# Kernel optimization log

Hardware: AMD Instinct MI355X
Metric: run time of the kernel (lower is better)

Reference implementation:

```python
import jax, jax.numpy as jnp
import numpy as np

# dims: batch, tokens, channels, heads, head_dim, slices, context_slices, context_dim
B, N, C, H, D, G, SC, DC = 2, 32768, 256, 8, 32, 32, 64, 32
EPS_SLICE = 1e-5


def _ln(x, g, b):
    m = x.mean(-1, keepdims=True)
    v = ((x - m) ** 2).mean(-1, keepdims=True)
    return (x - m) * jax.lax.rsqrt(v + 1e-5) * g + b


def setup_inputs() -> dict:
    key = jax.random.key(0)
    ks = jax.random.split(key, 16)
    w = lambda k, s: jax.random.normal(k, s, jnp.float32) * 0.02
    return dict(
        fx=jax.random.normal(ks[0], (B, N, C), jnp.float32),
        context=jax.random.normal(ks[1], (B, H, SC, DC), jnp.float32),
        ln1_g=jnp.ones((C,), jnp.float32), ln1_b=jnp.zeros((C,), jnp.float32),
        Wfx=w(ks[2], (C, H * D)), bfx=jnp.zeros((H * D,), jnp.float32),
        Wx=w(ks[3], (C, H * D)), bx=jnp.zeros((H * D,), jnp.float32),
        Wslice=w(ks[4], (D, G)), bslice=jnp.zeros((G,), jnp.float32),
        temperature=0.5 * jnp.ones((1, H, 1, 1), jnp.float32),
        Wq=w(ks[5], (D, D)), Wk=w(ks[6], (D, D)), Wv=w(ks[7], (D, D)),
        Wcq=w(ks[8], (D, D)), bcq=jnp.zeros((D,), jnp.float32),
        Wck=w(ks[9], (DC, D)), bck=jnp.zeros((D,), jnp.float32),
        Wcv=w(ks[10], (DC, D)), bcv=jnp.zeros((D,), jnp.float32),
        state_mixing=jnp.zeros((), jnp.float32),
        Wout=w(ks[11], (H * D, C)), bout=jnp.zeros((C,), jnp.float32),
        ln2_g=jnp.ones((C,), jnp.float32), ln2_b=jnp.zeros((C,), jnp.float32),
        Wm1=w(ks[12], (C, 4 * C)), bm1=jnp.zeros((4 * C,), jnp.float32),
        Wm2=w(ks[13], (4 * C, C)), bm2=jnp.zeros((C,), jnp.float32),
    )


def reference(fx, context, ln1_g, ln1_b, Wfx, bfx, Wx, bx, Wslice, bslice,
              temperature, Wq, Wk, Wv, Wcq, bcq, Wck, bck, Wcv, bcv,
              state_mixing, Wout, bout, ln2_g, ln2_b, Wm1, bm1, Wm2, bm2):
    # --- GALE attention on pre-normed input (Transolver physics attention + cross) ---
    x = _ln(fx, ln1_g, ln1_b)
    fxm = (x @ Wfx + bfx).reshape(B, N, H, D).transpose(0, 2, 1, 3)  # b h n d
    xm = (x @ Wx + bx).reshape(B, N, H, D).transpose(0, 2, 1, 3)    # b h n d
    # slice weights: softmax over slices with learnable per-head temperature
    sw = jax.nn.softmax((xm @ Wslice + bslice) / temperature, axis=-1)  # b h n g
    norm = sw.sum(2)  # b h g
    st = jnp.einsum('bhnd,bhng->bhgd', fxm, sw) / (norm + EPS_SLICE)[..., None]
    scale = D ** -0.5
    # self-attention among slice tokens (no bias on q/k/v)
    q, k, v = st @ Wq, st @ Wk, st @ Wv
    sattn = jax.nn.softmax(jnp.einsum('bhgd,bhmd->bhgm', q, k) * scale, axis=-1)
    self_tok = jnp.einsum('bhgm,bhmd->bhgd', sattn, v)
    # cross-attention of slice tokens onto geometry/global context
    cq = st @ Wcq + bcq
    ck = context @ Wck + bck
    cv = context @ Wcv + bcv
    cattn = jax.nn.softmax(jnp.einsum('bhgd,bhsd->bhgs', cq, ck) * scale, axis=-1)
    cross_tok = jnp.einsum('bhgs,bhsd->bhgd', cattn, cv)
    # sigmoid-gated mix
    mw = jax.nn.sigmoid(state_mixing)
    ost = mw * self_tok + (1.0 - mw) * cross_tok
    # de-slice back to tokens and output-project
    out = jnp.einsum('bhgd,bhng->bhnd', ost, sw)
    out = out.transpose(0, 2, 1, 3).reshape(B, N, H * D) @ Wout + bout
    fx = fx + out  # residual 1
    # --- MLP block ---
    h = _ln(fx, ln2_g, ln2_b)
    fx = fx + (jax.nn.gelu(h @ Wm1 + bm1, approximate=False) @ Wm2 + bm2)
    return fx
```

## Files before the change

kernel.cpp:

```cpp
#include <hip/hip_runtime.h>
#include <hip/hip_bf16.h>

#define BATCH 2
#define NTOK  32768
#define CH    256
#define NH    8
#define HDIM  32
#define NG    32
#define NSC   64
#define NDC   32

typedef __attribute__((ext_vector_type(8))) short short8v;
typedef __attribute__((ext_vector_type(4))) short short4v;
typedef __attribute__((ext_vector_type(4))) float f32x4;

static __device__ __forceinline__ short f2bf(float f) {
    __hip_bfloat16 h = __float2bfloat16(f);
    return __builtin_bit_cast(short, h);
}
static __device__ __forceinline__ float bf2f(short s) {
    return __bfloat162float(__builtin_bit_cast(__hip_bfloat16, s));
}

__global__ __launch_bounds__(256) void kconv_transpose(
    const float* __restrict__ in, __hip_bfloat16* __restrict__ out,
    int K, int N)
{
    __shared__ float t[32][33];
    const int nb = N >> 5;
    const int bk = blockIdx.x / nb;
    const int bn = blockIdx.x % nb;
    const int c = threadIdx.x & 31, r0 = threadIdx.x >> 5;
    #pragma unroll
    for (int i = 0; i < 4; ++i) {
        const int r = r0 + i * 8;
        t[r][c] = in[(long)(bk * 32 + r) * N + bn * 32 + c];
    }
    __syncthreads();
    #pragma unroll
    for (int i = 0; i < 4; ++i) {
        const int r = r0 + i * 8;
        out[(long)(bn * 32 + r) * K + bk * 32 + c] = __float2bfloat16(t[c][r]);
    }
}

__global__ __launch_bounds__(256) void kcomb(
    const float* __restrict__ Wx, const float* __restrict__ bx,
    const float* __restrict__ Wsl, const float* __restrict__ bsl,
    __hip_bfloat16* __restrict__ wcat2, float* __restrict__ bcomb)
{
    __shared__ float wcol[32];
    const int hc = blockIdx.x;
    const int h = hc >> 5, g = hc & 31;
    const int tid = threadIdx.x;
    if (tid < 32) wcol[tid] = Wsl[tid * 32 + g];
    __syncthreads();
    float a = 0.f;
    #pragma unroll
    for (int d = 0; d < 32; ++d) a += Wx[tid * 256 + h * 32 + d] * wcol[d];
    wcat2[(long)hc * 256 + tid] = __float2bfloat16(a);
    if (tid == 0) {
        float s = bsl[g];
        #pragma unroll
        for (int d = 0; d < 32; ++d) s += bx[h * 32 + d] * wcol[d];
        bcomb[hc] = s;
    }
}

__global__ __launch_bounds__(256, 2) void k1_mfma(
    const float* __restrict__ fx,
    const float* __restrict__ g1, const float* __restrict__ b1,
    const __hip_bfloat16* __restrict__ wcat,
    const float* __restrict__ bfx, const float* __restrict__ bcomb,
    const float* __restrict__ temp,
    __hip_bfloat16* __restrict__ fxm_o, __hip_bfloat16* __restrict__ sw_o)
{
    __shared__ __align__(16) char lds[65536];
    const int tid = threadIdx.x;
    const int lane = tid & 63, wid = tid >> 6;
    const long tok0 = (long)blockIdx.x * 64;
    const int col = lane & 15, kq = lane >> 4;
    const int swz = (col & 7) << 4;
    const int ep = ((kq * 16) ^ swz) & 48;
    const int e0 = (swz & 64) | ep;
    const int e1 = ((swz & 64) ^ 64) | ep;
    const int ab0 = col * 512 + e0, ab1 = col * 512 + e1;

    {
        const float4 gv = *reinterpret_cast<const float4*>(g1 + lane * 4);
        const float4 bv = *reinterpret_cast<const float4*>(b1 + lane * 4);
        for (int tt = 0; tt < 16; ++tt) {
            const int r = wid * 16 + tt;
            const float4 v = *reinterpret_cast<const float4*>(fx + (tok0 + r) * 256 + lane * 4);
            float s = v.x + v.y + v.z + v.w;
            float s2 = v.x * v.x + v.y * v.y + v.z * v.z + v.w * v.w;
            #pragma unroll
            for (int off = 32; off; off >>= 1) {
                s  += __shfl_xor(s,  off);
                s2 += __shfl_xor(s2, off);
            }
            const float mean = s * (1.f / 256.f);
            const float rs = rsqrtf(s2 * (1.f / 256.f) - mean * mean + 1e-5f);
            short4v o;
            o[0] = f2bf((v.x - mean) * rs * gv.x + bv.x);
            o[1] = f2bf((v.y - mean) * rs * gv.y + bv.y);
            o[2] = f2bf((v.z - mean) * rs * gv.z + bv.z);
            o[3] = f2bf((v.w - mean) * rs * gv.w + bv.w);
            const int addr = r * 512 + ((lane * 8) ^ ((r & 7) << 4));
            *reinterpret_cast<short4v*>(lds + addr) = o;
        }
    }
    __syncthreads();

    f32x4 acc[4][8];
    #pragma unroll
    for (int mt = 0; mt < 4; ++mt)
        #pragma unroll
        for (int nt = 0; nt < 8; ++nt) acc[mt][nt] = (f32x4){0.f, 0.f, 0.f, 0.f};

    const short* wp = reinterpret_cast<const short*>(wcat) + (wid * 128 + col) * 256 + kq * 8;
    #pragma unroll 2
    for (int j = 0; j < 4; ++j) {
        short8v a0[4], a1[4];
        #pragma unroll
        for (int mt = 0; mt < 4; ++mt) {
            a0[mt] = *reinterpret_cast<const short8v*>(lds + mt * 8192 + j * 128 + ab0);
            a1[mt] = *reinterpret_cast<const short8v*>(lds + mt * 8192 + j * 128 + ab1);
        }
        #pragma unroll
        for (int nt = 0; nt < 8; ++nt) {
            const short8v b0 = *reinterpret_cast<const short8v*>(wp + nt * 4096 + j * 64);
            const short8v b1 = *reinterpret_cast<const short8v*>(wp + nt * 4096 + j * 64 + 32);
            #pragma unroll
            for (int mt = 0; mt < 4; ++mt) {
                acc[mt][nt] = __builtin_amdgcn_mfma_f32_16x16x32_bf16(a0[mt], b0, acc[mt][nt], 0, 0, 0);
                acc[mt][nt] = __builtin_amdgcn_mfma_f32_16x16x32_bf16(a1[mt], b1, acc[mt][nt], 0, 0, 0);
            }
        }
    }
    __syncthreads();

    #pragma unroll
    for (int nt = 0; nt < 8; ++nt) {
        const int c = wid * 128 + nt * 16 + col;
        const float bb = (c < 256) ? bfx[c] : bcomb[c - 256];
        #pragma unroll
        for (int mt = 0; mt < 4; ++mt) {
            #pragma unroll
            for (int r = 0; r < 4; ++r) {
                const int row = mt * 16 + kq * 4 + r;
                const int byte = row * 1024 + ((c * 2) ^ ((row & 7) << 4));
                *reinterpret_cast<short*>(lds + byte) = f2bf(acc[mt][nt][r] + bb);
            }
        }
    }
    __syncthreads();

    #pragma unroll
    for (int it = 0; it < 8; ++it) {
        const int idx = it * 256 + tid;
        const int row = idx >> 5, ch = idx & 31;
        const short8v val = *reinterpret_cast<const short8v*>(
            lds + row * 1024 + ((ch * 16) ^ ((row & 7) << 4)));
        *reinterpret_cast<short8v*>(
            reinterpret_cast<short*>(fxm_o) + (tok0 + row) * 256 + ch * 8) = val;
    }

    #pragma unroll
    for (int pp = 0; pp < 2; ++pp) {
        const int p = pp * 256 + tid;
        const int t = p >> 3, h = p & 7;
        const float it_ = 1.f / temp[h];
        float lg[32];
        #pragma unroll
        for (int g = 0; g < 32; ++g) {
            const int byte = t * 1024 + (((256 + h * 32 + g) * 2) ^ ((t & 7) << 4));
            lg[g] = bf2f(*reinterpret_cast<const short*>(lds + byte)) * it_;
        }
        float mx = -1e30f;
        #pragma unroll
        for (int g = 0; g < 32; ++g) mx = fmaxf(mx, lg[g]);
        float ssum = 0.f;
        #pragma unroll
        for (int g = 0; g < 32; ++g) { lg[g] = __expf(lg[g] - mx); ssum += lg[g]; }
        const float inv = 1.f / ssum;
        #pragma unroll
        for (int g = 0; g < 32; ++g) {
            const int byte = t * 1024 + (((256 + h * 32 + g) * 2) ^ ((t & 7) << 4));
            *reinterpret_cast<short*>(lds + byte) = f2bf(lg[g] * inv);
        }
    }
    __syncthreads();

    #pragma unroll
    for (int it = 0; it < 8; ++it) {
        const int idx = it * 256 + tid;
        const int row = idx >> 5, ch = idx & 31;
        const short8v val = *reinterpret_cast<const short8v*>(
            lds + row * 1024 + ((512 + ch * 16) ^ ((row & 7) << 4)));
        *reinterpret_cast<short8v*>(
            reinterpret_cast<short*>(sw_o) + (tok0 + row) * 256 + ch * 8) = val;
    }
}

__global__ __launch_bounds__(256) void k2_st_partial(
    const __hip_bfloat16* __restrict__ fxm, const __hip_bfloat16* __restrict__ sw,
    float* __restrict__ pst, float* __restrict__ pn)
{
    __shared__ float psum[4][32][32];
    __shared__ float pns[4][32];
    const int tid = threadIdx.x, wid = tid >> 6, lane = tid & 63;
    const int blk = blockIdx.x;
    const int bh = blk >> 5, chunk = blk & 31;
    const int b = bh >> 3, h = bh & 7;
    const long rbase = (long)b * NTOK + (long)chunk * 1024 + wid * 256;
    const int gB = lane >> 3, dB = lane & 7;
    const short* sp = reinterpret_cast<const short*>(sw) + rbase * 256 + h * 32 + gB * 4;
    const short* fp = reinterpret_cast<const short*>(fxm) + rbase * 256 + h * 32 + dB * 4;

    float acc[4][4];
    float nacc[4];
    #pragma unroll
    for (int i = 0; i < 4; ++i) {
        nacc[i] = 0.f;
        #pragma unroll
        for (int j = 0; j < 4; ++j) acc[i][j] = 0.f;
    }

    #pragma unroll 4
    for (int r = 0; r < 256; ++r) {
        const short4v s4 = *reinterpret_cast<const short4v*>(sp + r * 256);
        const short4v f4 = *reinterpret_cast<const short4v*>(fp + r * 256);
        float sg[4], fd[4];
        #pragma unroll
        for (int i = 0; i < 4; ++i) { sg[i] = bf2f(s4[i]); fd[i] = bf2f(f4[i]); }
        #pragma unroll
        for (int gg = 0; gg < 4; ++gg) {
            nacc[gg] += sg[gg];
            #pragma unroll
            for (int dd = 0; dd < 4; ++dd) acc[gg][dd] += sg[gg] * fd[dd];
        }
    }

    #pragma unroll
    for (int gg = 0; gg < 4; ++gg) {
        #pragma unroll
        for (int dd = 0; dd < 4; ++dd)
            psum[wid][gB * 4 + gg][dB * 4 + dd] = acc[gg][dd];
        if (dB == 0) pns[wid][gB * 4 + gg] = nacc[gg];
    }
    __syncthreads();

    for (int i = tid; i < 1024; i += 256) {
        const int g = i >> 5, d = i & 31;
        pst[(long)blk * 1024 + i] =
            psum[0][g][d] + psum[1][g][d] + psum[2][g][d] + psum[3][g][d];
    }
    if (tid < 32)
        pn[blk * 32 + tid] = pns[0][tid] + pns[1][tid] + pns[2][tid] + pns[3][tid];
}

__global__ __launch_bounds__(256) void k3_slice_attn(
    const float* __restrict__ pst, const float* __restrict__ pn,
    const float* __restrict__ ctx,
    const float* __restrict__ Wq, const float* __restrict__ Wk, const float* __restrict__ Wv,
    const float* __restrict__ Wcq, const float* __restrict__ bcq,
    const float* __restrict__ Wck, const float* __restrict__ bck,
    const float* __restrict__ Wcv, const float* __restrict__ bcv,
    const float* __restrict__ mix, __hip_bfloat16* __restrict__ ostT_o)
{
    __shared__ float st[1024], qm[1024], km[1024], vm[1024], cqm[1024];
    __shared__ float ckm[2048], cvm[2048], attn[2048], stok[1024], nb[32];
    const int tid = threadIdx.x;
    const int bh = blockIdx.x;

    if (tid < 32) {
        float s = 0.f;
        for (int c = 0; c < 32; ++c) s += pn[(bh * 32 + c) * 32 + tid];
        nb[tid] = s;
    }
    __syncthreads();
    for (int i = tid; i < 1024; i += 256) {
        float s = 0.f;
        for (int c = 0; c < 32; ++c) s += pst[(long)(bh * 32 + c) * 1024 + i];
        st[i] = s / (nb[i >> 5] + 1e-5f);
    }
    __syncthreads();

    for (int i = tid; i < 1024; i += 256) {
        const int g = i >> 5, d = i & 31;
        float aq = 0.f, ak = 0.f, av = 0.f, ac = bcq[d];
        #pragma unroll
        for (int e = 0; e < 32; ++e) {
            const float s = st[g * 32 + e];
            aq += s * Wq[e * 32 + d];
            ak += s * Wk[e * 32 + d];
            av += s * Wv[e * 32 + d];
            ac += s * Wcq[e * 32 + d];
        }
        qm[i] = aq; km[i] = ak; vm[i] = av; cqm[i] = ac;
    }
    const float* cbp = ctx + (long)bh * (NSC * NDC);
    for (int i = tid; i < 2048; i += 256) {
        const int s_ = i >> 5, d = i & 31;
        float w1 = bck[d], w2 = bcv[d];
        #pragma unroll
        for (int e = 0; e < 32; ++e) {
            const float cval = cbp[s_ * 32 + e];
            w1 += cval * Wck[e * 32 + d];
            w2 += cval * Wcv[e * 32 + d];
        }
        ckm[i] = w1; cvm[i] = w2;
    }
    __syncthreads();

    const float scale = 0.17677669529663687f;
    for (int i = tid; i < 1024; i += 256) {
        const int g = i >> 5, m = i & 31;
        float a = 0.f;
        #pragma unroll
        for (int d = 0; d < 32; ++d) a += qm[g * 32 + d] * km[m * 32 + d];
        attn[i] = a * scale;
    }
    __syncthreads();
    if (tid < 32) {
        float mx = -1e30f;
        for (int m = 0; m < 32; ++m) mx = fmaxf(mx, attn[tid * 32 + m]);
        float s = 0.f;
        for (int m = 0; m < 32; ++m) { const float e = expf(attn[tid * 32 + m] - mx); attn[tid * 32 + m] = e; s += e; }
        const float inv = 1.f / s;
        for (int m = 0; m < 32; ++m) attn[tid * 32 + m] *= inv;
    }
    __syncthreads();
    for (int i = tid; i < 1024; i += 256) {
        const int g = i >> 5, d = i & 31;
        float a = 0.f;
        #pragma unroll
        for (int m = 0; m < 32; ++m) a += attn[g * 32 + m] * vm[m * 32 + d];
        stok[i] = a;
    }
    __syncthreads();
    for (int i = tid; i < 2048; i += 256) {
        const int g = i >> 6, s_ = i & 63;
        float a = 0.f;
        #pragma unroll
        for (int d = 0; d < 32; ++d) a += cqm[g * 32 + d] * ckm[s_ * 32 + d];
        attn[i] = a * scale;
    }
    __syncthreads();
    if (tid < 32) {
        float mx = -1e30f;
        for (int m = 0; m < 64; ++m) mx = fmaxf(mx, attn[tid * 64 + m]);
        float s = 0.f;
        for (int m = 0; m < 64; ++m) { const float e = expf(attn[tid * 64 + m] - mx); attn[tid * 64 + m] = e; s += e; }
        const float inv = 1.f / s;
        for (int m = 0; m < 64; ++m) attn[tid * 64 + m] *= inv;
    }
    __syncthreads();
    const float mw = 1.f / (1.f + expf(-mix[0]));
    for (int i = tid; i < 1024; i += 256) {
        const int g = i >> 5, d = i & 31;
        float a = 0.f;
        #pragma unroll
        for (int s_ = 0; s_ < 64; ++s_) a += attn[g * 64 + s_] * cvm[s_ * 32 + d];
        const float val = mw * stok[i] + (1.f - mw) * a;
        ostT_o[(long)bh * 1024 + d * 32 + g] = __float2bfloat16(val);
    }
}

__global__ __launch_bounds__(512, 4) void k45_fused(
    const __hip_bfloat16* __restrict__ sw, const __hip_bfloat16* __restrict__ ostT,
    const __hip_bfloat16* __restrict__ woutt, const float* __restrict__ bout,
    const float* __restrict__ fx,
    const float* __restrict__ g2, const float* __restrict__ b2,
    const __hip_bfloat16* __restrict__ w1t, const float* __restrict__ bm1,
    const __hip_bfloat16* __restrict__ w2t, const float* __restrict__ bm2,
    float* __restrict__ out)
{
    __shared__ __align__(16) char lds[65536];
    const int tid = threadIdx.x;
    const int lane = tid & 63, wid = tid >> 6;
    const long tok0 = (long)blockIdx.x * 64;
    const int b = (int)(tok0 >> 15);
    const int col = lane & 15, kq = lane >> 4;
    const int swz = (col & 7) << 4;
    const int ep = ((kq * 16) ^ swz) & 48;
    const int e0 = (swz & 64) | ep;
    const int e1 = ((swz & 64) ^ 64) | ep;
    const int ab0 = col * 512 + e0, ab1 = col * 512 + e1;
    const int cb0 = col * 256 + e0, cb1 = col * 256 + e1;

    #pragma unroll
    for (int it = 0; it < 4; ++it) {
        const int idx = it * 512 + tid;
        const int row = idx >> 5, ch = idx & 31;
        const short8v val = *reinterpret_cast<const short8v*>(
            reinterpret_cast<const short*>(sw) + (tok0 + row) * 256 + ch * 8);
        *reinterpret_cast<short8v*>(lds + row * 512 + ((ch * 16) ^ ((row & 7) << 4))) = val;
    }
    __syncthreads();

    {
        f32x4 accal[4][2];
        const int abh = col * 512 + (((wid * 64) | (kq * 16)) ^ swz);
        short8v a[4];
        #pragma unroll
        for (int mt = 0; mt < 4; ++mt)
            a[mt] = *reinterpret_cast<const short8v*>(lds + mt * 8192 + abh);
        #pragma unroll
        for (int nt = 0; nt < 2; ++nt) {
            const int d = nt * 16 + col;
            const short8v bfr = *reinterpret_cast<const short8v*>(
                reinterpret_cast<const short*>(ostT) + ((b * 8 + wid) * 32 + d) * 32 + kq * 8);
            #pragma unroll
            for (int mt = 0; mt < 4; ++mt) {
                accal[mt][nt] = (f32x4){0.f, 0.f, 0.f, 0.f};
                accal[mt][nt] = __builtin_amdgcn_mfma_f32_16x16x32_bf16(
                    a[mt], bfr, accal[mt][nt], 0, 0, 0);
            }
        }
        #pragma unroll
        for (int nt = 0; nt < 2; ++nt) {
            const int cc = wid * 32 + nt * 16 + col;
            #pragma unroll
            for (int mt = 0; mt < 4; ++mt) {
                #pragma unroll
                for (int r = 0; r < 4; ++r) {
                    const int row = mt * 16 + kq * 4 + r;
                    const int byte = 32768 + row * 512 + ((cc * 2) ^ ((row & 7) << 4));
                    *reinterpret_cast<short*>(lds + byte) = f2bf(accal[mt][nt][r]);
                }
            }
        }
    }
    __syncthreads();

    f32x4 acc[4][2];
    #pragma unroll
    for (int mt = 0; mt < 4; ++mt)
        #pragma unroll
        for (int nt = 0; nt < 2; ++nt) acc[mt][nt] = (f32x4){0.f, 0.f, 0.f, 0.f};

    {
        const short* wp = reinterpret_cast<const short*>(woutt) + (wid * 32 + col) * 256 + kq * 8;
        #pragma unroll 2
        for (int j = 0; j < 4; ++j) {
            short8v a0[4], a1[4];
            #pragma unroll
            for (int mt = 0; mt < 4; ++mt) {
                a0[mt] = *reinterpret_cast<const short8v*>(lds + 32768 + mt * 8192 + j * 128 + ab0);
                a1[mt] = *reinterpret_cast<const short8v*>(lds + 32768 + mt * 8192 + j * 128 + ab1);
            }
            #pragma unroll
            for (int nt = 0; nt < 2; ++nt) {
                const short8v b0 = *reinterpret_cast<const short8v*>(wp + nt * 4096 + j * 64);
                const short8v b1 = *reinterpret_cast<const short8v*>(wp + nt * 4096 + j * 64 + 32);
                #pragma unroll
                for (int mt = 0; mt < 4; ++mt) {
                    acc[mt][nt] = __builtin_amdgcn_mfma_f32_16x16x32_bf16(a0[mt], b0, acc[mt][nt], 0, 0, 0);
                    acc[mt][nt] = __builtin_amdgcn_mfma_f32_16x16x32_bf16(a1[mt], b1, acc[mt][nt], 0, 0, 0);
                }
            }
        }
    }

    __syncthreads();
    float* lf = reinterpret_cast<float*>(lds);
    #pragma unroll
    for (int nt = 0; nt < 2; ++nt) {
        const int c = wid * 32 + nt * 16 + col;
        const float bb = bout[c];
        #pragma unroll
        for (int mt = 0; mt < 4; ++mt) {
            #pragma unroll
            for (int r = 0; r < 4; ++r) {
                const int row = mt * 16 + kq * 4 + r;
                lf[row * 256 + c] = acc[mt][nt][r] + bb;
            }
        }
    }
    __syncthreads();

    f32x4 oa[8];
    short4v aout[8];
    {
        const float4 gv = *reinterpret_cast<const float4*>(g2 + lane * 4);
        const float4 bv = *reinterpret_cast<const float4*>(b2 + lane * 4);
        #pragma unroll
        for (int tt = 0; tt < 8; ++tt) {
            const int r = wid * 8 + tt;
            const float4 l4 = *reinterpret_cast<const float4*>(lf + r * 256 + lane * 4);
            const float4 f4 = *reinterpret_cast<const float4*>(fx + (tok0 + r) * 256 + lane * 4);
            const float vx = l4.x + f4.x, vy = l4.y + f4.y;
            const float vz = l4.z + f4.z, vw = l4.w + f4.w;
            oa[tt] = (f32x4){vx, vy, vz, vw};
            float s = vx + vy + vz + vw;
            float s2 = vx * vx + vy * vy + vz * vz + vw * vw;
            #pragma unroll
            for (int off = 32; off; off >>= 1) {
                s  += __shfl_xor(s,  off);
                s2 += __shfl_xor(s2, off);
            }
            const float mean = s * (1.f / 256.f);
            const float rs = rsqrtf(s2 * (1.f / 256.f) - mean * mean + 1e-5f);
            aout[tt][0] = f2bf((vx - mean) * rs * gv.x + bv.x);
            aout[tt][1] = f2bf((vy - mean) * rs * gv.y + bv.y);
            aout[tt][2] = f2bf((vz - mean) * rs * gv.z + bv.z);
            aout[tt][3] = f2bf((vw - mean) * rs * gv.w + bv.w);
        }
    }
    __syncthreads();
    #pragma unroll
    for (int tt = 0; tt < 8; ++tt) {
        const int r = wid * 8 + tt;
        const int addr = r * 512 + ((lane * 8) ^ ((r & 7) << 4));
        *reinterpret_cast<short4v*>(lds + addr) = aout[tt];
    }
    __syncthreads();

    const int n0 = wid * 32;
    const int h0 = wid * 16;
    const short* w1s = reinterpret_cast<const short*>(w1t) + (h0 + col) * 256 + kq * 8;
    const short* w2s = reinterpret_cast<const short*>(w2t) + (n0 + col) * 1024 + kq * 8;

    f32x4 accO[4][2];
    #pragma unroll
    for (int mt = 0; mt < 4; ++mt)
        #pragma unroll
        for (int nt = 0; nt < 2; ++nt) accO[mt][nt] = (f32x4){0.f, 0.f, 0.f, 0.f};

    for (int ch = 0; ch < 8; ++ch) {
        f32x4 accP[4];
        #pragma unroll
        for (int mt = 0; mt < 4; ++mt) accP[mt] = (f32x4){0.f, 0.f, 0.f, 0.f};

        #pragma unroll 2
        for (int j = 0; j < 4; ++j) {
            const short8v b0 = *reinterpret_cast<const short8v*>(w1s + ch * 32768 + j * 64);
            const short8v b1 = *reinterpret_cast<const short8v*>(w1s + ch * 32768 + j * 64 + 32);
            #pragma unroll
            for (int mt = 0; mt < 4; ++mt) {
                const short8v a0 = *reinterpret_cast<const short8v*>(lds + mt * 8192 + j * 128 + ab0);
                const short8v a1 = *reinterpret_cast<const short8v*>(lds + mt * 8192 + j * 128 + ab1);
                accP[mt] = __builtin_amdgcn_mfma_f32_16x16x32_bf16(a0, b0, accP[mt], 0, 0, 0);
                accP[mt] = __builtin_amdgcn_mfma_f32_16x16x32_bf16(a1, b1, accP[mt], 0, 0, 0);
            }
        }

        __syncthreads();
        {
            const float b1v = bm1[ch * 128 + h0 + col];
            const int k2i2 = (h0 + col) * 2;
            #pragma unroll
            for (int mt = 0; mt < 4; ++mt) {
                #pragma unroll
                for (int r = 0; r < 4; ++r) {
                    float m = accP[mt][r] + b1v;
                    const float u = __builtin_fmaf(0.044715f * m, m * m, m);
                    const float e = __expf(-1.5957691216057308f * u);
                    m = m * __builtin_amdgcn_rcpf(1.f + e);
                    const int row = mt * 16 + kq * 4 + r;
                    const int byte = 32768 + row * 256 + (k2i2 ^ ((row & 7) << 4));
                    *reinterpret_cast<short*>(lds + byte) = f2bf(m);
                }
            }
        }
        __syncthreads();

        #pragma unroll 2
        for (int j = 0; j < 2; ++j) {
            short8v b20[2], b21[2];
            #pragma unroll
            for (int nt = 0; nt < 2; ++nt) {
                b20[nt] = *reinterpret_cast<const short8v*>(w2s + nt * 16384 + ch * 128 + j * 64);
                b21[nt] = *reinterpret_cast<const short8v*>(w2s + nt * 16384 + ch * 128 + j * 64 + 32);
            }
            #pragma unroll
            for (int mt = 0; mt < 4; ++mt) {
                const short8v x0 = *reinterpret_cast<const short8v*>(lds + 32768 + mt * 4096 + j * 128 + cb0);
                const short8v x1 = *reinterpret_cast<const short8v*>(lds + 32768 + mt * 4096 + j * 128 + cb1);
                #pragma unroll
                for (int nt = 0; nt < 2; ++nt) {
                    accO[mt][nt] = __builtin_amdgcn_mfma_f32_16x16x32_bf16(x0, b20[nt], accO[mt][nt], 0, 0, 0);
                    accO[mt][nt] = __builtin_amdgcn_mfma_f32_16x16x32_bf16(x1, b21[nt], accO[mt][nt], 0, 0, 0);
                }
            }
        }
    }

    __syncthreads();
    #pragma unroll
    for (int nt = 0; nt < 2; ++nt) {
        const int c = n0 + nt * 16 + col;
        const float b2v = bm2[c];
        #pragma unroll
        for (int mt = 0; mt < 4; ++mt) {
            #pragma unroll
            for (int r = 0; r < 4; ++r) {
                const int row = mt * 16 + kq * 4 + r;
                lf[row * 256 + c] = accO[mt][nt][r] + b2v;
            }
        }
    }
    __syncthreads();
    #pragma unroll
    for (int tt = 0; tt < 8; ++tt) {
        const int r = wid * 8 + tt;
        const float4 m4 = *reinterpret_cast<const float4*>(lf + r * 256 + lane * 4);
        float4 o;
        o.x = oa[tt][0] + m4.x;
        o.y = oa[tt][1] + m4.y;
        o.z = oa[tt][2] + m4.z;
        o.w = oa[tt][3] + m4.w;
        *reinterpret_cast<float4*>(out + (tok0 + r) * 256 + lane * 4) = o;
    }
}

extern "C" void kernel_launch(void* const* d_in, const int* in_sizes, int n_in,
                              void* d_out, int out_size, void* d_ws, size_t ws_size,
                              hipStream_t stream)
{
    const float* fx   = (const float*)d_in[0];
    const float* ctx  = (const float*)d_in[1];
    const float* g1   = (const float*)d_in[2];
    const float* b1   = (const float*)d_in[3];
    const float* Wfx  = (const float*)d_in[4];
    const float* bfx  = (const float*)d_in[5];
    const float* Wx   = (const float*)d_in[6];
    const float* bx   = (const float*)d_in[7];
    const float* Wsl  = (const float*)d_in[8];
    const float* bsl  = (const float*)d_in[9];
    const float* temp = (const float*)d_in[10];
    const float* Wq   = (const float*)d_in[11];
    const float* Wk   = (const float*)d_in[12];
    const float* Wv   = (const float*)d_in[13];
    const float* Wcq  = (const float*)d_in[14];
    const float* bcq  = (const float*)d_in[15];
    const float* Wck  = (const float*)d_in[16];
    const float* bck  = (const float*)d_in[17];
    const float* Wcv  = (const float*)d_in[18];
    const float* bcv  = (const float*)d_in[19];
    const float* mix  = (const float*)d_in[20];
    const float* Wout = (const float*)d_in[21];
    const float* bout = (const float*)d_in[22];
    const float* g2   = (const float*)d_in[23];
    const float* b2   = (const float*)d_in[24];
    const float* Wm1  = (const float*)d_in[25];
    const float* bm1  = (const float*)d_in[26];
    const float* Wm2  = (const float*)d_in[27];
    const float* bm2  = (const float*)d_in[28];
    float* out = (float*)d_out;

    char* ws = (char*)d_ws;
    __hip_bfloat16* fxm  = (__hip_bfloat16*)ws;
    __hip_bfloat16* sw   = (__hip_bfloat16*)(ws + (size_t)33554432);
    float* pst = (float*)(ws + (size_t)67108864);
    float* pn  = (float*)(ws + (size_t)69206016);
    __hip_bfloat16* ostT  = (__hip_bfloat16*)(ws + (size_t)69271552);
    __hip_bfloat16* wcat  = (__hip_bfloat16*)(ws + (size_t)69304320);
    __hip_bfloat16* woutt = (__hip_bfloat16*)(ws + (size_t)69566464);
    __hip_bfloat16* w1t   = (__hip_bfloat16*)(ws + (size_t)69697536);
    __hip_bfloat16* w2t   = (__hip_bfloat16*)(ws + (size_t)70221824);
    float* bcomb          = (float*)(ws + (size_t)70746112);

    kconv_transpose<<<64,  256, 0, stream>>>(Wfx, wcat,  256, 256);
    kcomb<<<256, 256, 0, stream>>>(Wx, bx, Wsl, bsl, wcat + 65536, bcomb);
    kconv_transpose<<<64,  256, 0, stream>>>(Wout, woutt, 256, 256);
    kconv_transpose<<<256, 256, 0, stream>>>(Wm1, w1t,    256, 1024);
    kconv_transpose<<<256, 256, 0, stream>>>(Wm2, w2t,    1024, 256);

    k1_mfma<<<1024, 256, 0, stream>>>(fx, g1, b1, wcat, bfx, bcomb, temp,
                                      fxm, sw);
    k2_st_partial<<<512, 256, 0, stream>>>(fxm, sw, pst, pn);
    k3_slice_attn<<<16, 256, 0, stream>>>(pst, pn, ctx, Wq, Wk, Wv,
                                          Wcq, bcq, Wck, bck, Wcv, bcv, mix, ostT);
    k45_fused<<<1024, 512, 0, stream>>>(sw, ostT, woutt, bout, fx,
                                        g2, b2, w1t, bm1, w2t, bm2, out);
}
```

Baseline: 329.3 us.

## Widen MLP hidden chunk to 256 and spill residual to output buffer

The fused MLP kernel now processes the 1024-wide hidden dimension in 4 chunks of 256 instead of 8 chunks of 128. Each wave computes two 16-column tiles of the first GEMM, reusing the A fragments it loads from LDS across both. The hidden activations are stored with a new swizzled LDS layout that the second GEMM reads with the same addressing as the first. The residual sum (fx + attention output) is written to global output early and re-read at the end instead of being held in 32 registers, which lowers register pressure at the cost of extra global traffic.

```diff
diff --git a/kernel.cpp b/kernel.cpp
--- a/kernel.cpp
+++ b/kernel.cpp
@@ -388,7 +388,6 @@
     const int e0 = (swz & 64) | ep;
     const int e1 = ((swz & 64) ^ 64) | ep;
     const int ab0 = col * 512 + e0, ab1 = col * 512 + e1;
-    const int cb0 = col * 256 + e0, cb1 = col * 256 + e1;
 
     #pragma unroll
     for (int it = 0; it < 4; ++it) {
@@ -481,7 +480,6 @@
     }
     __syncthreads();
 
-    f32x4 oa[8];
     short4v aout[8];
     {
         const float4 gv = *reinterpret_cast<const float4*>(g2 + lane * 4);
@@ -491,11 +489,12 @@
             const int r = wid * 8 + tt;
             const float4 l4 = *reinterpret_cast<const float4*>(lf + r * 256 + lane * 4);
             const float4 f4 = *reinterpret_cast<const float4*>(fx + (tok0 + r) * 256 + lane * 4);
-            const float vx = l4.x + f4.x, vy = l4.y + f4.y;
-            const float vz = l4.z + f4.z, vw = l4.w + f4.w;
-            oa[tt] = (f32x4){vx, vy, vz, vw};
-            float s = vx + vy + vz + vw;
-            float s2 = vx * vx + vy * vy + vz * vz + vw * vw;
+            float4 oa;
+            oa.x = l4.x + f4.x; oa.y = l4.y + f4.y;
+            oa.z = l4.z + f4.z; oa.w = l4.w + f4.w;
+            *reinterpret_cast<float4*>(out + (tok0 + r) * 256 + lane * 4) = oa;
+            float s = oa.x + oa.y + oa.z + oa.w;
+            float s2 = oa.x * oa.x + oa.y * oa.y + oa.z * oa.z + oa.w * oa.w;
             #pragma unroll
             for (int off = 32; off; off >>= 1) {
                 s  += __shfl_xor(s,  off);
@@ -503,10 +502,10 @@
             }
             const float mean = s * (1.f / 256.f);
             const float rs = rsqrtf(s2 * (1.f / 256.f) - mean * mean + 1e-5f);
-            aout[tt][0] = f2bf((vx - mean) * rs * gv.x + bv.x);
-            aout[tt][1] = f2bf((vy - mean) * rs * gv.y + bv.y);
-            aout[tt][2] = f2bf((vz - mean) * rs * gv.z + bv.z);
-            aout[tt][3] = f2bf((vw - mean) * rs * gv.w + bv.w);
+            aout[tt][0] = f2bf((oa.x - mean) * rs * gv.x + bv.x);
+            aout[tt][1] = f2bf((oa.y - mean) * rs * gv.y + bv.y);
+            aout[tt][2] = f2bf((oa.z - mean) * rs * gv.z + bv.z);
+            aout[tt][3] = f2bf((oa.w - mean) * rs * gv.w + bv.w);
         }
     }
     __syncthreads();
@@ -519,9 +518,9 @@
     __syncthreads();
 
     const int n0 = wid * 32;
-    const int h0 = wid * 16;
-    const short* w1s = reinterpret_cast<const short*>(w1t) + (h0 + col) * 256 + kq * 8;
+    const short* w1s = reinterpret_cast<const short*>(w1t) + (n0 + col) * 256 + kq * 8;
     const short* w2s = reinterpret_cast<const short*>(w2t) + (n0 + col) * 1024 + kq * 8;
+    const int gsw = (kq & 1) << 6;
 
     f32x4 accO[4][2];
     #pragma unroll
@@ -529,38 +528,50 @@
         #pragma unroll
         for (int nt = 0; nt < 2; ++nt) accO[mt][nt] = (f32x4){0.f, 0.f, 0.f, 0.f};
 
-    for (int ch = 0; ch < 8; ++ch) {
-        f32x4 accP[4];
-        #pragma unroll
-        for (int mt = 0; mt < 4; ++mt) accP[mt] = (f32x4){0.f, 0.f, 0.f, 0.f};
+    for (int ch = 0; ch < 4; ++ch) {
+        f32x4 accP[4][2];
+        #pragma unroll
+        for (int mt = 0; mt < 4; ++mt)
+            #pragma unroll
+            for (int nt = 0; nt < 2; ++nt) accP[mt][nt] = (f32x4){0.f, 0.f, 0.f, 0.f};
 
         #pragma unroll 2
         for (int j = 0; j < 4; ++j) {
-            const short8v b0 = *reinterpret_cast<const short8v*>(w1s + ch * 32768 + j * 64);
-            const short8v b1 = *reinterpret_cast<const short8v*>(w1s + ch * 32768 + j * 64 + 32);
+            short8v a0[4], a1[4];
             #pragma unroll
             for (int mt = 0; mt < 4; ++mt) {
-                const short8v a0 = *reinterpret_cast<const short8v*>(lds + mt * 8192 + j * 128 + ab0);
-                const short8v a1 = *reinterpret_cast<const short8v*>(lds + mt * 8192 + j * 128 + ab1);
-                accP[mt] = __builtin_amdgcn_mfma_f32_16x16x32_bf16(a0, b0, accP[mt], 0, 0, 0);
-                accP[mt] = __builtin_amdgcn_mfma_f32_16x16x32_bf16(a1, b1, accP[mt], 0, 0, 0);
+                a0[mt] = *reinterpret_cast<const short8v*>(lds + mt * 8192 + j * 128 + ab0);
+                a1[mt] = *reinterpret_cast<const short8v*>(lds + mt * 8192 + j * 128 + ab1);
+            }
+            #pragma unroll
+            for (int nt = 0; nt < 2; ++nt) {
+                const short8v b0 = *reinterpret_cast<const short8v*>(
+                    w1s + ch * 65536 + nt * 4096 + j * 64);
+                const short8v b1 = *reinterpret_cast<const short8v*>(
+                    w1s + ch * 65536 + nt * 4096 + j * 64 + 32);
+                #pragma unroll
+                for (int mt = 0; mt < 4; ++mt) {
+                    accP[mt][nt] = __builtin_amdgcn_mfma_f32_16x16x32_bf16(a0[mt], b0, accP[mt][nt], 0, 0, 0);
+                    accP[mt][nt] = __builtin_amdgcn_mfma_f32_16x16x32_bf16(a1[mt], b1, accP[mt][nt], 0, 0, 0);
+                }
             }
         }
 
         __syncthreads();
-        {
-            const float b1v = bm1[ch * 128 + h0 + col];
-            const int k2i2 = (h0 + col) * 2;
+        #pragma unroll
+        for (int nt = 0; nt < 2; ++nt) {
+            const float b1v = bm1[ch * 256 + n0 + nt * 16 + col];
+            const int k2i2 = (n0 + nt * 16 + col) * 2;
             #pragma unroll
             for (int mt = 0; mt < 4; ++mt) {
                 #pragma unroll
                 for (int r = 0; r < 4; ++r) {
-                    float m = accP[mt][r] + b1v;
+                    float m = accP[mt][nt][r] + b1v;
                     const float u = __builtin_fmaf(0.044715f * m, m * m, m);
                     const float e = __expf(-1.5957691216057308f * u);
                     m = m * __builtin_amdgcn_rcpf(1.f + e);
-                    const int row = mt * 16 + kq * 4 + r;
-                    const int byte = 32768 + row * 256 + (k2i2 ^ ((row & 7) << 4));
+                    const int byte = 32768 + kq * 2048 + mt * 8192 + r * 512
+                                     + (k2i2 ^ (gsw + r * 16));
                     *reinterpret_cast<short*>(lds + byte) = f2bf(m);
                 }
             }
@@ -568,21 +579,23 @@
         __syncthreads();
 
         #pragma unroll 2
-        for (int j = 0; j < 2; ++j) {
-            short8v b20[2], b21[2];
+        for (int j = 0; j < 4; ++j) {
+            short8v a0[4], a1[4];
+            #pragma unroll
+            for (int mt = 0; mt < 4; ++mt) {
+                a0[mt] = *reinterpret_cast<const short8v*>(lds + 32768 + mt * 8192 + j * 128 + ab0);
+                a1[mt] = *reinterpret_cast<const short8v*>(lds + 32768 + mt * 8192 + j * 128 + ab1);
+            }
             #pragma unroll
             for (int nt = 0; nt < 2; ++nt) {
-                b20[nt] = *reinterpret_cast<const short8v*>(w2s + nt * 16384 + ch * 128 + j * 64);
-                b21[nt] = *reinterpret_cast<const short8v*>(w2s + nt * 16384 + ch * 128 + j * 64 + 32);
-            }
-            #pragma unroll
-            for (int mt = 0; mt < 4; ++mt) {
-                const short8v x0 = *reinterpret_cast<const short8v*>(lds + 32768 + mt * 4096 + j * 128 + cb0);
-                const short8v x1 = *reinterpret_cast<const short8v*>(lds + 32768 + mt * 4096 + j * 128 + cb1);
+                const short8v b0 = *reinterpret_cast<const short8v*>(
+                    w2s + nt * 16384 + ch * 256 + j * 64);
+                const short8v b1 = *reinterpret_cast<const short8v*>(
+                    w2s + nt * 16384 + ch * 256 + j * 64 + 32);
                 #pragma unroll
-                for (int nt = 0; nt < 2; ++nt) {
-                    accO[mt][nt] = __builtin_amdgcn_mfma_f32_16x16x32_bf16(x0, b20[nt], accO[mt][nt], 0, 0, 0);
-                    accO[mt][nt] = __builtin_amdgcn_mfma_f32_16x16x32_bf16(x1, b21[nt], accO[mt][nt], 0, 0, 0);
+                for (int mt = 0; mt < 4; ++mt) {
+                    accO[mt][nt] = __builtin_amdgcn_mfma_f32_16x16x32_bf16(a0[mt], b0, accO[mt][nt], 0, 0, 0);
+                    accO[mt][nt] = __builtin_amdgcn_mfma_f32_16x16x32_bf16(a1[mt], b1, accO[mt][nt], 0, 0, 0);
                 }
             }
         }
@@ -607,12 +620,12 @@
     for (int tt = 0; tt < 8; ++tt) {
         const int r = wid * 8 + tt;
         const float4 m4 = *reinterpret_cast<const float4*>(lf + r * 256 + lane * 4);
+        const long gidx = (tok0 + r) * 256 + lane * 4;
+        const float4 oa = *reinterpret_cast<const float4*>(out + gidx);
         float4 o;
-        o.x = oa[tt][0] + m4.x;
-        o.y = oa[tt][1] + m4.y;
-        o.z = oa[tt][2] + m4.z;
-        o.w = oa[tt][3] + m4.w;
-        *reinterpret_cast<float4*>(out + (tok0 + r) * 256 + lane * 4) = o;
+        o.x = oa.x + m4.x; o.y = oa.y + m4.y;
+        o.z = oa.z + m4.z; o.w = oa.w + m4.w;
+        *reinterpret_cast<float4*>(out + gidx) = o;
     }
 }
 
```

Measured after the change: 321.4 us. 2.4% less time.

## Widen k1 and k2 to 512 threads, merge weight transposes, tune k45 occupancy

Applied to the files above, without the earlier changes.

Four weight-transpose launches become one kernel that dispatches on block index. k1_mfma and k2_st_partial move from 256 to 512 threads per block, halving each wave's share of the output tiles and rows, which raises wave-level parallelism and lowers per-thread register pressure. k45_fused gets an explicit waves-per-EU attribute and its inner GEMM loops drop from unroll 2 to unroll 1, to hold occupancy. The risks are more LDS reduction traffic in k2 and less instruction-level overlap in k45 from the reduced unrolling.

```diff
diff --git a/kernel.cpp b/kernel.cpp
--- a/kernel.cpp
+++ b/kernel.cpp
@@ -22,15 +22,15 @@
     return __bfloat162float(__builtin_bit_cast(__hip_bfloat16, s));
 }
 
-__global__ __launch_bounds__(256) void kconv_transpose(
+static __device__ __forceinline__ void transpose_tile(
     const float* __restrict__ in, __hip_bfloat16* __restrict__ out,
-    int K, int N)
+    int K, int N, int blk, int tid)
 {
     __shared__ float t[32][33];
     const int nb = N >> 5;
-    const int bk = blockIdx.x / nb;
-    const int bn = blockIdx.x % nb;
-    const int c = threadIdx.x & 31, r0 = threadIdx.x >> 5;
+    const int bk = blk / nb;
+    const int bn = blk % nb;
+    const int c = tid & 31, r0 = tid >> 5;
     #pragma unroll
     for (int i = 0; i < 4; ++i) {
         const int r = r0 + i * 8;
@@ -42,6 +42,19 @@
         const int r = r0 + i * 8;
         out[(long)(bn * 32 + r) * K + bk * 32 + c] = __float2bfloat16(t[c][r]);
     }
+}
+
+__global__ __launch_bounds__(256) void kconv_all(
+    const float* __restrict__ Wfx, __hip_bfloat16* __restrict__ wcat,
+    const float* __restrict__ Wout, __hip_bfloat16* __restrict__ woutt,
+    const float* __restrict__ Wm1, __hip_bfloat16* __restrict__ w1t,
+    const float* __restrict__ Wm2, __hip_bfloat16* __restrict__ w2t)
+{
+    const int b = blockIdx.x, tid = threadIdx.x;
+    if (b < 64)            transpose_tile(Wfx,  wcat,  256, 256,  b,        tid);
+    else if (b < 128)      transpose_tile(Wout, woutt, 256, 256,  b - 64,   tid);
+    else if (b < 384)      transpose_tile(Wm1,  w1t,   256, 1024, b - 128,  tid);
+    else                   transpose_tile(Wm2,  w2t,   1024, 256, b - 384,  tid);
 }
 
 __global__ __launch_bounds__(256) void kcomb(
@@ -67,7 +80,7 @@
     }
 }
 
-__global__ __launch_bounds__(256, 2) void k1_mfma(
+__global__ __launch_bounds__(512, 4) void k1_mfma(
     const float* __restrict__ fx,
     const float* __restrict__ g1, const float* __restrict__ b1,
     const __hip_bfloat16* __restrict__ wcat,
@@ -89,8 +102,9 @@
     {
         const float4 gv = *reinterpret_cast<const float4*>(g1 + lane * 4);
         const float4 bv = *reinterpret_cast<const float4*>(b1 + lane * 4);
-        for (int tt = 0; tt < 16; ++tt) {
-            const int r = wid * 16 + tt;
+        #pragma unroll
+        for (int tt = 0; tt < 8; ++tt) {
+            const int r = wid * 8 + tt;
             const float4 v = *reinterpret_cast<const float4*>(fx + (tok0 + r) * 256 + lane * 4);
             float s = v.x + v.y + v.z + v.w;
             float s2 = v.x * v.x + v.y * v.y + v.z * v.z + v.w * v.w;
@@ -112,13 +126,14 @@
     }
     __syncthreads();
 
-    f32x4 acc[4][8];
+    const int n0 = wid * 64;
+    f32x4 acc[4][4];
     #pragma unroll
     for (int mt = 0; mt < 4; ++mt)
         #pragma unroll
-        for (int nt = 0; nt < 8; ++nt) acc[mt][nt] = (f32x4){0.f, 0.f, 0.f, 0.f};
-
-    const short* wp = reinterpret_cast<const short*>(wcat) + (wid * 128 + col) * 256 + kq * 8;
+        for (int nt = 0; nt < 4; ++nt) acc[mt][nt] = (f32x4){0.f, 0.f, 0.f, 0.f};
+
+    const short* wp = reinterpret_cast<const short*>(wcat) + (n0 + col) * 256 + kq * 8;
     #pragma unroll 2
     for (int j = 0; j < 4; ++j) {
         short8v a0[4], a1[4];
@@ -128,7 +143,7 @@
             a1[mt] = *reinterpret_cast<const short8v*>(lds + mt * 8192 + j * 128 + ab1);
         }
         #pragma unroll
-        for (int nt = 0; nt < 8; ++nt) {
+        for (int nt = 0; nt < 4; ++nt) {
             const short8v b0 = *reinterpret_cast<const short8v*>(wp + nt * 4096 + j * 64);
             const short8v b1 = *reinterpret_cast<const short8v*>(wp + nt * 4096 + j * 64 + 32);
             #pragma unroll
@@ -141,8 +156,8 @@
     __syncthreads();
 
     #pragma unroll
-    for (int nt = 0; nt < 8; ++nt) {
-        const int c = wid * 128 + nt * 16 + col;
+    for (int nt = 0; nt < 4; ++nt) {
+        const int c = n0 + nt * 16 + col;
         const float bb = (c < 256) ? bfx[c] : bcomb[c - 256];
         #pragma unroll
         for (int mt = 0; mt < 4; ++mt) {
@@ -157,8 +172,8 @@
     __syncthreads();
 
     #pragma unroll
-    for (int it = 0; it < 8; ++it) {
-        const int idx = it * 256 + tid;
+    for (int it = 0; it < 4; ++it) {
+        const int idx = it * 512 + tid;
         const int row = idx >> 5, ch = idx & 31;
         const short8v val = *reinterpret_cast<const short8v*>(
             lds + row * 1024 + ((ch * 16) ^ ((row & 7) << 4)));
@@ -166,10 +181,8 @@
             reinterpret_cast<short*>(fxm_o) + (tok0 + row) * 256 + ch * 8) = val;
     }
 
-    #pragma unroll
-    for (int pp = 0; pp < 2; ++pp) {
-        const int p = pp * 256 + tid;
-        const int t = p >> 3, h = p & 7;
+    {
+        const int t = tid >> 3, h = tid & 7;
         const float it_ = 1.f / temp[h];
         float lg[32];
         #pragma unroll
@@ -193,8 +206,8 @@
     __syncthreads();
 
     #pragma unroll
-    for (int it = 0; it < 8; ++it) {
-        const int idx = it * 256 + tid;
+    for (int it = 0; it < 4; ++it) {
+        const int idx = it * 512 + tid;
         const int row = idx >> 5, ch = idx & 31;
         const short8v val = *reinterpret_cast<const short8v*>(
             lds + row * 1024 + ((512 + ch * 16) ^ ((row & 7) << 4)));
@@ -203,17 +216,17 @@
     }
 }
 
-__global__ __launch_bounds__(256) void k2_st_partial(
+__global__ __launch_bounds__(512) void k2_st_partial(
     const __hip_bfloat16* __restrict__ fxm, const __hip_bfloat16* __restrict__ sw,
     float* __restrict__ pst, float* __restrict__ pn)
 {
-    __shared__ float psum[4][32][32];
-    __shared__ float pns[4][32];
+    __shared__ float psum[8][32][32];
+    __shared__ float pns[8][32];
     const int tid = threadIdx.x, wid = tid >> 6, lane = tid & 63;
     const int blk = blockIdx.x;
     const int bh = blk >> 5, chunk = blk & 31;
     const int b = bh >> 3, h = bh & 7;
-    const long rbase = (long)b * NTOK + (long)chunk * 1024 + wid * 256;
+    const long rbase = (long)b * NTOK + (long)chunk * 1024 + wid * 128;
     const int gB = lane >> 3, dB = lane & 7;
     const short* sp = reinterpret_cast<const short*>(sw) + rbase * 256 + h * 32 + gB * 4;
     const short* fp = reinterpret_cast<const short*>(fxm) + rbase * 256 + h * 32 + dB * 4;
@@ -228,7 +241,7 @@
     }
 
     #pragma unroll 4
-    for (int r = 0; r < 256; ++r) {
+    for (int r = 0; r < 128; ++r) {
         const short4v s4 = *reinterpret_cast<const short4v*>(sp + r * 256);
         const short4v f4 = *reinterpret_cast<const short4v*>(fp + r * 256);
         float sg[4], fd[4];
@@ -251,13 +264,19 @@
     }
     __syncthreads();
 
-    for (int i = tid; i < 1024; i += 256) {
+    for (int i = tid; i < 1024; i += 512) {
         const int g = i >> 5, d = i & 31;
-        pst[(long)blk * 1024 + i] =
-            psum[0][g][d] + psum[1][g][d] + psum[2][g][d] + psum[3][g][d];
-    }
-    if (tid < 32)
-        pn[blk * 32 + tid] = pns[0][tid] + pns[1][tid] + pns[2][tid] + pns[3][tid];
+        float s = 0.f;
+        #pragma unroll
+        for (int w = 0; w < 8; ++w) s += psum[w][g][d];
+        pst[(long)blk * 1024 + i] = s;
+    }
+    if (tid < 32) {
+        float s = 0.f;
+        #pragma unroll
+        for (int w = 0; w < 8; ++w) s += pns[w][tid];
+        pn[blk * 32 + tid] = s;
+    }
 }
 
 __global__ __launch_bounds__(256) void k3_slice_attn(
@@ -368,7 +387,8 @@
     }
 }
 
-__global__ __launch_bounds__(512, 4) void k45_fused(
+__global__ __launch_bounds__(512, 4) __attribute__((amdgpu_waves_per_eu(4, 4)))
+void k45_fused(
     const __hip_bfloat16* __restrict__ sw, const __hip_bfloat16* __restrict__ ostT,
     const __hip_bfloat16* __restrict__ woutt, const float* __restrict__ bout,
     const float* __restrict__ fx,
@@ -534,7 +554,7 @@
         #pragma unroll
         for (int mt = 0; mt < 4; ++mt) accP[mt] = (f32x4){0.f, 0.f, 0.f, 0.f};
 
-        #pragma unroll 2
+        #pragma unroll 1
         for (int j = 0; j < 4; ++j) {
             const short8v b0 = *reinterpret_cast<const short8v*>(w1s + ch * 32768 + j * 64);
             const short8v b1 = *reinterpret_cast<const short8v*>(w1s + ch * 32768 + j * 64 + 32);
@@ -567,7 +587,7 @@
         }
         __syncthreads();
 
-        #pragma unroll 2
+        #pragma unroll 1
         for (int j = 0; j < 2; ++j) {
             short8v b20[2], b21[2];
             #pragma unroll
@@ -663,15 +683,12 @@
     __hip_bfloat16* w2t   = (__hip_bfloat16*)(ws + (size_t)70221824);
     float* bcomb          = (float*)(ws + (size_t)70746112);
 
-    kconv_transpose<<<64,  256, 0, stream>>>(Wfx, wcat,  256, 256);
+    kconv_all<<<640, 256, 0, stream>>>(Wfx, wcat, Wout, woutt, Wm1, w1t, Wm2, w2t);
     kcomb<<<256, 256, 0, stream>>>(Wx, bx, Wsl, bsl, wcat + 65536, bcomb);
-    kconv_transpose<<<64,  256, 0, stream>>>(Wout, woutt, 256, 256);
-    kconv_transpose<<<256, 256, 0, stream>>>(Wm1, w1t,    256, 1024);
-    kconv_transpose<<<256, 256, 0, stream>>>(Wm2, w2t,    1024, 256);
-
-    k1_mfma<<<1024, 256, 0, stream>>>(fx, g1, b1, wcat, bfx, bcomb, temp,
+
+    k1_mfma<<<1024, 512, 0, stream>>>(fx, g1, b1, wcat, bfx, bcomb, temp,
                                       fxm, sw);
-    k2_st_partial<<<512, 256, 0, stream>>>(fxm, sw, pst, pn);
+    k2_st_partial<<<512, 512, 0, stream>>>(fxm, sw, pst, pn);
     k3_slice_attn<<<16, 256, 0, stream>>>(pst, pn, ctx, Wq, Wk, Wv,
                                           Wcq, bcq, Wck, bck, Wcv, bcv, mix, ostT);
     k45_fused<<<1024, 512, 0, stream>>>(sw, ostT, woutt, bout, fx,
```

New measurement: 316.2 us. -4.0%, faster.
